# Performance work log

Measured on AMD Instinct MI355X. Metric: run time of the kernel, lower is better.

Reference implementation:

```python
import jax, jax.numpy as jnp
import numpy as np

LOCAL_MAX_DISP = 12
STRIDE = 1


def setup_inputs() -> dict:
    key = jax.random.key(0)
    k1, k2 = jax.random.split(key)
    B, H, W, C = 8, 256, 512, 32
    feat_l = jax.random.normal(k1, (B, H, W, C), dtype=jnp.float32)
    feat_r = jax.random.normal(k2, (B, H, W, C), dtype=jnp.float32)
    return {"feat_l": feat_l, "feat_r": feat_r}


def reference(feat_l, feat_r):
    # Faithful translation of CostVolume2D.call:
    # For disparity i = d*stride:
    #   cost[:, :, w, d] = sum_c |feat_l[:, :, w, c] - feat_r[:, :, w-i, c]|  for w >= i
    #   cost[:, :, w, d] = sum_c |feat_l[:, :, w, c]|                         for w <  i
    # The w < i case equals L1(feat_l - 0), so zero-padding feat_r on the left
    # by i columns reproduces both branches in one fused abs-diff reduction.
    B, H, W, C = feat_l.shape
    n_disp = LOCAL_MAX_DISP // STRIDE  # 12

    def cost_at(i):
        # shift feat_r right by i columns, zero-fill on the left  -> [B, H, W, C]
        shifted_r = jnp.pad(feat_r, ((0, 0), (0, 0), (i, 0), (0, 0)))[:, :, :W, :]
        return jnp.sum(jnp.abs(feat_l - shifted_r), axis=-1)  # [B, H, W]

    # small fixed loop over disparities (n_disp = 12), vectorized over B,H,W,C
    cost = jnp.stack([cost_at(d * STRIDE) for d in range(n_disp)], axis=-1)
    return cost  # [B, H, W, n_disp]
```

## Files before the change

kernel.cpp:

```cpp
#include <hip/hip_runtime.h>


constexpr int Wd   = 512;
constexpr int ND   = 12;
constexpr int NCOL = 272;

typedef float vfloat4 __attribute__((ext_vector_type(4)));

__device__ __forceinline__ float l1_4(float4 a, float4 b) {
    return fabsf(a.x - b.x) + fabsf(a.y - b.y) + fabsf(a.z - b.z) + fabsf(a.w - b.w);
}

__global__ __launch_bounds__(256) void cost_volume_kernel(
    const float* __restrict__ fl,
    const float* __restrict__ fr,
    float* __restrict__ out)
{
    __shared__ float4 lds4[8 * NCOL];

    const int t    = threadIdx.x;
    const int wave = t >> 6;
    const int lane = t & 63;
    const int wstart = (blockIdx.x & 1) * 256;
    const int bh     = blockIdx.x >> 1;
    const float* fr_row = fr + (size_t)bh * Wd * 32;

    const int q0 = 2 * wave;
    #pragma unroll
    for (int run = 0; run < 5; ++run) {
        const int colr = run * 64 + lane;
        int col = wstart - 11 + colr;
        col = max(col, 0);
        if (run < 4 || lane < 267 - 256) {
            #pragma unroll
            for (int dq = 0; dq < 2; ++dq) {
                const int q = q0 + dq;
                __builtin_amdgcn_global_load_lds(
                    (const __attribute__((address_space(1))) void*)(fr_row + (size_t)col * 32 + q * 4),
                    (__attribute__((address_space(3))) void*)(lds4 + q * NCOL + run * 64 + lane),
                    16, 0, 0);
            }
        }
    }

    const int w = wstart + t;
    const size_t pix = (size_t)bh * Wd + w;
    const float4* lp = reinterpret_cast<const float4*>(fl) + pix * 8;
    float4 L[8];
    #pragma unroll
    for (int q = 0; q < 8; ++q) L[q] = lp[q];

    float lsum = 0.f;
    #pragma unroll
    for (int q = 0; q < 8; ++q)
        lsum += fabsf(L[q].x) + fabsf(L[q].y) + fabsf(L[q].z) + fabsf(L[q].w);

    __syncthreads();

    float res[ND];
    #pragma unroll
    for (int d = 0; d < ND; ++d) res[d] = 0.f;

    #pragma unroll
    for (int q = 0; q < 8; ++q) {
        const float4 Lq = L[q];
        const float4* base = &lds4[q * NCOL + t];
        #pragma unroll
        for (int d = 0; d < ND; ++d) {
            res[d] += l1_4(Lq, base[11 - d]);
        }
    }

    #pragma unroll
    for (int d = 0; d < ND; ++d)
        if (w < d) res[d] = lsum;

    vfloat4* op = reinterpret_cast<vfloat4*>(out + pix * ND);
    vfloat4 o0 = {res[0], res[1], res[2],  res[3]};
    vfloat4 o1 = {res[4], res[5], res[6],  res[7]};
    vfloat4 o2 = {res[8], res[9], res[10], res[11]};
    __builtin_nontemporal_store(o0, op + 0);
    __builtin_nontemporal_store(o1, op + 1);
    __builtin_nontemporal_store(o2, op + 2);
}

extern "C" void kernel_launch(void* const* d_in, const int* in_sizes, int n_in,
                              void* d_out, int out_size, void* d_ws, size_t ws_size,
                              hipStream_t stream)
{
    const float* fl = (const float*)d_in[0];
    const float* fr = (const float*)d_in[1];
    float* out = (float*)d_out;

    const int grid = 8 * 256 * 2;
    cost_volume_kernel<<<grid, 256, 0, stream>>>(fl, fr, out);
}
```

Baseline: 57.81 us.

## Give each wave a private LDS window to replace the block barrier with a waitcnt

Each wave now loads its own 76-column halo window of the right features into a private LDS region, instead of the block sharing one 267-column window. This lets the block-wide __syncthreads be replaced by a per-wave s_waitcnt vmcnt(0) plus a scheduling barrier, so waves no longer wait on each other. The cost is redundant halo loads (11 extra columns per 64 instead of per 256) and larger LDS use per block, which may reduce occupancy. Relying on vmcnt alone to order the LDS-direct loads within a wave is an assumption about how global_load_lds completes.

Measured after the change: 64.92 us. +12.3%, slower.

```diff
diff --git a/kernel.cpp b/kernel.cpp
--- a/kernel.cpp
+++ b/kernel.cpp
@@ -1,14 +1,17 @@
 #include <hip/hip_runtime.h>
 
 
-constexpr int Wd   = 512;
-constexpr int ND   = 12;
-constexpr int NCOL = 272;
+constexpr int ND     = 12;
+constexpr int NCOL   = 76;
+constexpr int WCHUNK = 8 * NCOL;
 
 typedef float vfloat4 __attribute__((ext_vector_type(4)));
 
 __device__ __forceinline__ float l1_4(float4 a, float4 b) {
     return fabsf(a.x - b.x) + fabsf(a.y - b.y) + fabsf(a.z - b.z) + fabsf(a.w - b.w);
+}
+__device__ __forceinline__ float abs4(float4 a) {
+    return fabsf(a.x) + fabsf(a.y) + fabsf(a.z) + fabsf(a.w);
 }
 
 __global__ __launch_bounds__(256) void cost_volume_kernel(
@@ -16,46 +19,41 @@
     const float* __restrict__ fr,
     float* __restrict__ out)
 {
-    __shared__ float4 lds4[8 * NCOL];
+    __shared__ float4 lds4[4 * WCHUNK];
 
     const int t    = threadIdx.x;
     const int wave = t >> 6;
     const int lane = t & 63;
-    const int wstart = (blockIdx.x & 1) * 256;
-    const int bh     = blockIdx.x >> 1;
-    const float* fr_row = fr + (size_t)bh * Wd * 32;
+    const int bh   = blockIdx.x >> 1;
+    const int seg  = (blockIdx.x & 1) * 256 + wave * 64;
+    const float* fr_row = fr + (size_t)bh * 512 * 32;
+    float4* wb = lds4 + wave * WCHUNK;
 
-    const int q0 = 2 * wave;
     #pragma unroll
-    for (int run = 0; run < 5; ++run) {
-        const int colr = run * 64 + lane;
-        int col = wstart - 11 + colr;
-        col = max(col, 0);
-        if (run < 4 || lane < 267 - 256) {
-            #pragma unroll
-            for (int dq = 0; dq < 2; ++dq) {
-                const int q = q0 + dq;
-                __builtin_amdgcn_global_load_lds(
-                    (const __attribute__((address_space(1))) void*)(fr_row + (size_t)col * 32 + q * 4),
-                    (__attribute__((address_space(3))) void*)(lds4 + q * NCOL + run * 64 + lane),
-                    16, 0, 0);
-            }
+    for (int it = 0; it < 10; ++it) {
+        const int g = it * 64 + lane;
+        if (it < 9 || lane < WCHUNK - 576) {
+            const int q    = g / NCOL;
+            const int colr = g - q * NCOL;
+            int col = seg - 11 + colr;
+            col = min(max(col, 0), 511);
+            __builtin_amdgcn_global_load_lds(
+                (const __attribute__((address_space(1))) void*)(fr_row + (size_t)col * 32 + q * 4),
+                (__attribute__((address_space(3))) void*)(wb + g),
+                16, 0, 0);
         }
     }
 
-    const int w = wstart + t;
-    const size_t pix = (size_t)bh * Wd + w;
+    const int w = seg + lane;
+    const size_t pix = (size_t)bh * 512 + w;
     const float4* lp = reinterpret_cast<const float4*>(fl) + pix * 8;
     float4 L[8];
-    #pragma unroll
-    for (int q = 0; q < 8; ++q) L[q] = lp[q];
-
     float lsum = 0.f;
     #pragma unroll
-    for (int q = 0; q < 8; ++q)
-        lsum += fabsf(L[q].x) + fabsf(L[q].y) + fabsf(L[q].z) + fabsf(L[q].w);
+    for (int q = 0; q < 8; ++q) { L[q] = lp[q]; lsum += abs4(L[q]); }
 
-    __syncthreads();
+    asm volatile("s_waitcnt vmcnt(0)" ::: "memory");
+    __builtin_amdgcn_sched_barrier(0);
 
     float res[ND];
     #pragma unroll
@@ -64,10 +62,10 @@
     #pragma unroll
     for (int q = 0; q < 8; ++q) {
         const float4 Lq = L[q];
-        const float4* base = &lds4[q * NCOL + t];
+        const float4* base = wb + q * NCOL + lane + 11;
         #pragma unroll
         for (int d = 0; d < ND; ++d) {
-            res[d] += l1_4(Lq, base[11 - d]);
+            res[d] += l1_4(Lq, base[-d]);
         }
     }
 
```

## Process four tiles per block with double-buffered LDS prefetch of right features

Applied to the files above, without the earlier changes.

Each block now handles four consecutive row-half tiles, staging the next tile's right-feature window into a second LDS buffer via async global-to-LDS loads while computing the current tile. Manual vmcnt waits and barriers replace the single syncthreads. The aim is to hide load latency and reduce block launch overhead, at the cost of doubled LDS use, fewer blocks and possibly lower occupancy.

Result: slower. 66.86 us (+15.7%).

```diff
diff --git a/kernel.cpp b/kernel.cpp
--- a/kernel.cpp
+++ b/kernel.cpp
@@ -1,14 +1,42 @@
 #include <hip/hip_runtime.h>
 
 
-constexpr int Wd   = 512;
 constexpr int ND   = 12;
 constexpr int NCOL = 272;
+constexpr int TCH  = 8 * NCOL;
+constexpr int NT   = 4;
 
 typedef float vfloat4 __attribute__((ext_vector_type(4)));
 
 __device__ __forceinline__ float l1_4(float4 a, float4 b) {
     return fabsf(a.x - b.x) + fabsf(a.y - b.y) + fabsf(a.z - b.z) + fabsf(a.w - b.w);
+}
+__device__ __forceinline__ float abs4(float4 a) {
+    return fabsf(a.x) + fabsf(a.y) + fabsf(a.z) + fabsf(a.w);
+}
+
+__device__ __forceinline__ void stage_tile(const float* __restrict__ fr, int tile,
+                                           float4* dst, int wave, int lane)
+{
+    const int bh     = tile >> 1;
+    const int wstart = (tile & 1) * 256;
+    const float* fr_row = fr + (size_t)bh * 512 * 32;
+    #pragma unroll
+    for (int run = 0; run < 5; ++run) {
+        const int colr = run * 64 + lane;
+        int col = wstart - 11 + colr;
+        col = max(col, 0);
+        if (run < 4 || lane < 11) {
+            #pragma unroll
+            for (int dq = 0; dq < 2; ++dq) {
+                const int q = 2 * wave + dq;
+                __builtin_amdgcn_global_load_lds(
+                    (const __attribute__((address_space(1))) void*)(fr_row + (size_t)col * 32 + q * 4),
+                    (__attribute__((address_space(3))) void*)(dst + q * NCOL + colr),
+                    16, 0, 0);
+            }
+        }
+    }
 }
 
 __global__ __launch_bounds__(256) void cost_volume_kernel(
@@ -16,72 +44,67 @@
     const float* __restrict__ fr,
     float* __restrict__ out)
 {
-    __shared__ float4 lds4[8 * NCOL];
+    __shared__ float4 lds4[2 * TCH];
 
     const int t    = threadIdx.x;
     const int wave = t >> 6;
     const int lane = t & 63;
-    const int wstart = (blockIdx.x & 1) * 256;
-    const int bh     = blockIdx.x >> 1;
-    const float* fr_row = fr + (size_t)bh * Wd * 32;
+    const int tile0 = blockIdx.x * NT;
 
-    const int q0 = 2 * wave;
-    #pragma unroll
-    for (int run = 0; run < 5; ++run) {
-        const int colr = run * 64 + lane;
-        int col = wstart - 11 + colr;
-        col = max(col, 0);
-        if (run < 4 || lane < 267 - 256) {
+    stage_tile(fr, tile0, lds4, wave, lane);
+
+    #pragma unroll 1
+    for (int tt = 0; tt < NT; ++tt) {
+        const int tile = tile0 + tt;
+        const int bh   = tile >> 1;
+        const int w    = (tile & 1) * 256 + t;
+        const size_t pix = (size_t)bh * 512 + w;
+
+        const float4* lp = reinterpret_cast<const float4*>(fl) + pix * 8;
+        float4 L[8];
+        #pragma unroll
+        for (int q = 0; q < 8; ++q) L[q] = lp[q];
+
+        if (tt + 1 < NT)
+            stage_tile(fr, tile + 1, lds4 + ((tt + 1) & 1) * TCH, wave, lane);
+
+        if (tt + 1 < NT) {
+            asm volatile("s_waitcnt vmcnt(10)" ::: "memory");
+        } else {
+            asm volatile("s_waitcnt vmcnt(0)" ::: "memory");
+        }
+        __builtin_amdgcn_s_barrier();
+
+        const float4* buf = lds4 + (tt & 1) * TCH;
+        float lsum = 0.f;
+        float res[ND];
+        #pragma unroll
+        for (int d = 0; d < ND; ++d) res[d] = 0.f;
+
+        #pragma unroll
+        for (int q = 0; q < 8; ++q) {
+            const float4 Lq = L[q];
+            lsum += abs4(Lq);
+            const float4* base = buf + q * NCOL + t;
             #pragma unroll
-            for (int dq = 0; dq < 2; ++dq) {
-                const int q = q0 + dq;
-                __builtin_amdgcn_global_load_lds(
-                    (const __attribute__((address_space(1))) void*)(fr_row + (size_t)col * 32 + q * 4),
-                    (__attribute__((address_space(3))) void*)(lds4 + q * NCOL + run * 64 + lane),
-                    16, 0, 0);
-            }
+            for (int d = 0; d < ND; ++d)
+                res[d] += l1_4(Lq, base[11 - d]);
         }
+
+        #pragma unroll
+        for (int d = 0; d < ND; ++d)
+            if (w < d) res[d] = lsum;
+
+        vfloat4* op = reinterpret_cast<vfloat4*>(out + pix * ND);
+        vfloat4 o0 = {res[0], res[1], res[2],  res[3]};
+        vfloat4 o1 = {res[4], res[5], res[6],  res[7]};
+        vfloat4 o2 = {res[8], res[9], res[10], res[11]};
+        __builtin_nontemporal_store(o0, op + 0);
+        __builtin_nontemporal_store(o1, op + 1);
+        __builtin_nontemporal_store(o2, op + 2);
+
+        __builtin_amdgcn_s_barrier();
     }
-
-    const int w = wstart + t;
-    const size_t pix = (size_t)bh * Wd + w;
-    const float4* lp = reinterpret_cast<const float4*>(fl) + pix * 8;
-    float4 L[8];
-    #pragma unroll
-    for (int q = 0; q < 8; ++q) L[q] = lp[q];
-
-    float lsum = 0.f;
-    #pragma unroll
-    for (int q = 0; q < 8; ++q)
-        lsum += fabsf(L[q].x) + fabsf(L[q].y) + fabsf(L[q].z) + fabsf(L[q].w);
-
-    __syncthreads();
-
-    float res[ND];
-    #pragma unroll
-    for (int d = 0; d < ND; ++d) res[d] = 0.f;
-
-    #pragma unroll
-    for (int q = 0; q < 8; ++q) {
-        const float4 Lq = L[q];
-        const float4* base = &lds4[q * NCOL + t];
-        #pragma unroll
-        for (int d = 0; d < ND; ++d) {
-            res[d] += l1_4(Lq, base[11 - d]);
-        }
-    }
-
-    #pragma unroll
-    for (int d = 0; d < ND; ++d)
-        if (w < d) res[d] = lsum;
-
-    vfloat4* op = reinterpret_cast<vfloat4*>(out + pix * ND);
-    vfloat4 o0 = {res[0], res[1], res[2],  res[3]};
-    vfloat4 o1 = {res[4], res[5], res[6],  res[7]};
-    vfloat4 o2 = {res[8], res[9], res[10], res[11]};
-    __builtin_nontemporal_store(o0, op + 0);
-    __builtin_nontemporal_store(o1, op + 1);
-    __builtin_nontemporal_store(o2, op + 2);
 }
 
 extern "C" void kernel_launch(void* const* d_in, const int* in_sizes, int n_in,
@@ -92,6 +115,6 @@
     const float* fr = (const float*)d_in[1];
     float* out = (float*)d_out;
 
-    const int grid = 8 * 256 * 2;
+    const int grid = 8 * 256 * 2 / NT;
     cost_volume_kernel<<<grid, 256, 0, stream>>>(fl, fr, out);
 }
```
